# Kernel tuning notes

Hardware: AMD Instinct MI355X
Metric: run time of the kernel (lower is better)

The kernel has to match this reference:

```python
import jax, jax.numpy as jnp
import numpy as np

B, N, D, M = 8, 8192, 256, 2  # M from init_kwargs


def setup_inputs() -> dict:
    key = jax.random.key(0)
    ks = jax.random.split(key, 10)
    g_names = ['G_l_ii', 'G_l_ij', 'G_l_ji', 'G_l_jj', 'G_u_ii', 'G_u_ij', 'G_u_ji', 'G_u_jj']
    inp = {'input': jax.random.normal(ks[0], (B, N, D), dtype=jnp.float32)}
    for i, name in enumerate(g_names):
        inp[name] = jax.random.normal(ks[1 + i], (B, N - 1), dtype=jnp.float32)
    inp['Diag'] = jax.random.normal(ks[9], (B, N), dtype=jnp.float32)
    inp['transform'] = 1
    return inp


def _banded_sweep(x, a0, b0, lo, dm, hi, aL, bL):
    # One tridiagonal Givens sweep over axis 1 of x [B,N,D].
    # row 0:       a0*x[0]   + b0*x[1]
    # rows 1..N-2: lo*x[i-1] + dm*x[i] + hi*x[i+1]
    # row N-1:     aL*x[N-2] + bL*x[N-1]
    n = x.shape[1]
    y0 = a0[:, None, None] * x[:, 0:1] + b0[:, None, None] * x[:, 1:2]
    ym = (lo[:, :, None] * x[:, :-2]
          + dm[:, :, None] * x[:, 1:n - 1]
          + hi[:, :, None] * x[:, 2:])
    yl = aL[:, None, None] * x[:, n - 2:n - 1] + bL[:, None, None] * x[:, n - 1:n]
    return jnp.concatenate([y0, ym, yl], axis=1)


def _forward(x, gl_ii, gl_ij, gl_ji, gl_jj, gu_ii, gu_ij, gu_ji, gu_jj, diag, transform):
    b, n, d = x.shape
    if transform:
        # stride permutation (only defined for even N in the original)
        x = x.reshape(b, n // M, M, d).transpose(0, 2, 1, 3).reshape(b, n, d)
    else:
        x = diag[:, :, None] * x
    # upper sweep -> Y
    y = _banded_sweep(
        x,
        gu_ii[:, 0], gu_ij[:, 0],
        gu_ji[:, :-1], gu_jj[:, :-1] * gu_ii[:, 1:], gu_jj[:, :-1] * gu_ij[:, 1:],
        gu_ji[:, n - 2], gu_jj[:, n - 2])
    # lower sweep -> Z
    z = _banded_sweep(
        y,
        gl_ii[:, 0], gl_ij[:, 0],
        gl_ii[:, 1:] * gl_ji[:, :-1], gl_ii[:, 1:] * gl_jj[:, :-1], gl_ij[:, 1:],
        gl_ji[:, n - 2], gl_jj[:, n - 2])
    if transform:
        z = diag[:, :, None] * z
    else:
        z = z.reshape(b, n // M, M, d).transpose(0, 2, 1, 3).reshape(b, n, d)
    return z


def reference(input, G_l_ii, G_l_ij, G_l_ji, G_l_jj, G_u_ii, G_u_ij, G_u_ji, G_u_jj, Diag, transform):
    return _forward(input, G_l_ii, G_l_ij, G_l_ji, G_l_jj,
                    G_u_ii, G_u_ij, G_u_ji, G_u_jj, Diag, transform)
```

## Files before the change

### kernel.cpp

```cpp
#include <hip/hip_runtime.h>

#define NN 8192
#define DD 256
#define NH (NN / 2)
#define BB 8
#define RPW 8
#define WPB 4
#define RPB (RPW * WPB)
#define SROWS (RPB + 4)
#define NBLK (BB * NN / RPB)
#define CPX (NBLK / 8)

__device__ __forceinline__ float4 f4_scale(float s, float4 v) {
    return make_float4(s * v.x, s * v.y, s * v.z, s * v.w);
}
__device__ __forceinline__ float4 f4_fma(float s, float4 v, float4 a) {
    return make_float4(fmaf(s, v.x, a.x), fmaf(s, v.y, a.y),
                       fmaf(s, v.z, a.z), fmaf(s, v.w, a.w));
}

__global__ __launch_bounds__(256) void dhhp_kernel(
    const float* __restrict__ x,
    const float* __restrict__ gl_ii, const float* __restrict__ gl_ij,
    const float* __restrict__ gl_ji, const float* __restrict__ gl_jj,
    const float* __restrict__ gu_ii, const float* __restrict__ gu_ij,
    const float* __restrict__ gu_ji, const float* __restrict__ gu_jj,
    const float* __restrict__ diag, const int* __restrict__ transform,
    float* __restrict__ out)
{
    __shared__ float smem[SROWS * DD];

    const int bid = blockIdx.x;
    const int swz = (bid & 7) * CPX + (bid >> 3);
    const int b   = swz >> 8;
    const int j0b = (swz & 255) << 5;
    const int w   = __builtin_amdgcn_readfirstlane(threadIdx.x >> 6);
    const int col = (threadIdx.x & 63) << 2;
    const int tr  = *transform;

    const float* xb  = x    + (size_t)b * NN * DD;
    const float* db  = diag + (size_t)b * NN;
    const float* uii = gu_ii + (size_t)b * (NN - 1);
    const float* uij = gu_ij + (size_t)b * (NN - 1);
    const float* uji = gu_ji + (size_t)b * (NN - 1);
    const float* ujj = gu_jj + (size_t)b * (NN - 1);
    const float* lii = gl_ii + (size_t)b * (NN - 1);
    const float* lij = gl_ij + (size_t)b * (NN - 1);
    const float* lji = gl_ji + (size_t)b * (NN - 1);
    const float* ljj = gl_jj + (size_t)b * (NN - 1);
    float* ob = out + (size_t)b * NN * DD;

    #pragma unroll
    for (int q = 0; q < SROWS / WPB; ++q) {
        const int s  = w + q * WPB;
        const int i  = j0b - 2 + s;
        const int ic = i < 0 ? 0 : (i > NN - 1 ? NN - 1 : i);
        const int r  = tr ? ((ic < NH) ? (ic << 1) : (((ic - NH) << 1) | 1)) : ic;
        const float* gp = xb + (size_t)r * DD + col;
        float*       lp = smem + s * DD;
        __builtin_amdgcn_global_load_lds(
            (const __attribute__((address_space(1))) void*)gp,
            (__attribute__((address_space(3))) void*)lp, 16, 0, 0);
    }
    __syncthreads();

    const int j0 = j0b + (w << 3);

    auto xRow = [&](int i) -> float4 {
        const int s = i - (j0b - 2);
        float4 v = *reinterpret_cast<const float4*>(smem + s * DD + col);
        if (!tr) {
            const int ic = i < 0 ? 0 : (i > NN - 1 ? NN - 1 : i);
            v = f4_scale(db[ic], v);
        }
        return v;
    };
    auto yInner = [&](int i, float4 xm, float4 xc, float4 xp) -> float4 {
        float lo  = uji[i - 1];
        float cjj = ujj[i - 1];
        float dm  = cjj * uii[i];
        float hi  = cjj * uij[i];
        float4 r = f4_scale(lo, xm);
        r = f4_fma(dm, xc, r);
        r = f4_fma(hi, xp, r);
        return r;
    };
    auto yAny = [&](int i, float4 xm, float4 xc, float4 xp) -> float4 {
        int ic = i < 0 ? 0 : (i > NN - 1 ? NN - 1 : i);
        if (ic == 0)      return f4_fma(uii[0], xc, f4_scale(uij[0], xp));
        if (ic == NN - 1) return f4_fma(uji[NN - 2], xm, f4_scale(ujj[NN - 2], xc));
        return yInner(ic, xm, xc, xp);
    };
    auto zInner = [&](int j, float4 ym, float4 yc, float4 yp) -> float4 {
        float ci = lii[j];
        float lo = ci * lji[j - 1];
        float dm = ci * ljj[j - 1];
        float hi = lij[j];
        float4 r = f4_scale(lo, ym);
        r = f4_fma(dm, yc, r);
        r = f4_fma(hi, yp, r);
        return r;
    };
    auto zAny = [&](int j, float4 ym, float4 yc, float4 yp) -> float4 {
        if (j == 0)      return f4_fma(lii[0], yc, f4_scale(lij[0], yp));
        if (j == NN - 1) return f4_fma(lji[NN - 2], ym, f4_scale(ljj[NN - 2], yc));
        return zInner(j, ym, yc, yp);
    };
    auto storeRow = [&](int j, float4 z) {
        int jo;
        float4 o;
        if (tr) { o = f4_scale(db[j], z); jo = j; }
        else    { o = z; jo = (j & 1) ? (NH + (j >> 1)) : (j >> 1); }
        *reinterpret_cast<float4*>(ob + (size_t)jo * DD + col) = o;
    };

    float4 xr[RPW + 4];
    float4 yr[RPW + 2];

    const bool interior = (j0 >= 2) && (j0 <= NN - RPW - 2);

    if (interior) {
        #pragma unroll
        for (int t = 0; t < RPW + 4; ++t) xr[t] = xRow(j0 - 2 + t);
        #pragma unroll
        for (int t = 0; t < RPW + 2; ++t)
            yr[t] = yInner(j0 - 1 + t, xr[t], xr[t + 1], xr[t + 2]);
        #pragma unroll
        for (int t = 0; t < RPW; ++t)
            storeRow(j0 + t, zInner(j0 + t, yr[t], yr[t + 1], yr[t + 2]));
    } else {
        #pragma unroll
        for (int t = 0; t < RPW + 4; ++t) xr[t] = xRow(j0 - 2 + t);
        #pragma unroll
        for (int t = 0; t < RPW + 2; ++t)
            yr[t] = yAny(j0 - 1 + t, xr[t], xr[t + 1], xr[t + 2]);
        #pragma unroll
        for (int t = 0; t < RPW; ++t)
            storeRow(j0 + t, zAny(j0 + t, yr[t], yr[t + 1], yr[t + 2]));
    }
}

extern "C" void kernel_launch(void* const* d_in, const int* in_sizes, int n_in,
                              void* d_out, int out_size, void* d_ws, size_t ws_size,
                              hipStream_t stream) {
    const float* x     = (const float*)d_in[0];
    const float* gl_ii = (const float*)d_in[1];
    const float* gl_ij = (const float*)d_in[2];
    const float* gl_ji = (const float*)d_in[3];
    const float* gl_jj = (const float*)d_in[4];
    const float* gu_ii = (const float*)d_in[5];
    const float* gu_ij = (const float*)d_in[6];
    const float* gu_ji = (const float*)d_in[7];
    const float* gu_jj = (const float*)d_in[8];
    const float* diag  = (const float*)d_in[9];
    const int* transform = (const int*)d_in[10];
    float* out = (float*)d_out;

    dim3 grid(NBLK);
    dim3 block(256);
    hipLaunchKernelGGL(dhhp_kernel, grid, block, 0, stream,
                       x, gl_ii, gl_ij, gl_ji, gl_jj,
                       gu_ii, gu_ij, gu_ji, gu_jj, diag, transform, out);
}
```

Baseline: 31.41 us.

## Process two row tiles per block with overlapped LDS staging via partial waitcnt

Each block now handles two 32-row tiles, issuing global-to-LDS loads for both up front into double-buffered shared memory. It then waits only for the first tile's loads (partial vmcnt) before computing it, so the second tile's loads overlap with the first tile's compute. This halves the grid and doubles LDS per block, which may reduce occupancy. It also relies on hand-counted vmcnt values being correct relative to the loads and stores the compiler emits.

Measured after the change: 38.67 us. +23.1%, slower.

```diff
diff --git a/kernel.cpp b/kernel.cpp
--- a/kernel.cpp
+++ b/kernel.cpp
@@ -6,9 +6,11 @@
 #define BB 8
 #define RPW 8
 #define WPB 4
-#define RPB (RPW * WPB)
-#define SROWS (RPB + 4)
-#define NBLK (BB * NN / RPB)
+#define RPT (RPW * WPB)
+#define TPB 2
+#define SROWS (RPT + 4)
+#define LPW (SROWS / WPB)
+#define NBLK (BB * NN / (RPT * TPB))
 #define CPX (NBLK / 8)
 
 __device__ __forceinline__ float4 f4_scale(float s, float4 v) {
@@ -28,12 +30,12 @@
     const float* __restrict__ diag, const int* __restrict__ transform,
     float* __restrict__ out)
 {
-    __shared__ float smem[SROWS * DD];
+    __shared__ float smem[TPB * SROWS * DD];
 
     const int bid = blockIdx.x;
     const int swz = (bid & 7) * CPX + (bid >> 3);
-    const int b   = swz >> 8;
-    const int j0b = (swz & 255) << 5;
+    const int b   = swz >> 7;
+    const int t0  = (swz & 127) << 6;
     const int w   = __builtin_amdgcn_readfirstlane(threadIdx.x >> 6);
     const int col = (threadIdx.x & 63) << 2;
     const int tr  = *transform;
@@ -50,94 +52,112 @@
     const float* ljj = gl_jj + (size_t)b * (NN - 1);
     float* ob = out + (size_t)b * NN * DD;
 
-    #pragma unroll
-    for (int q = 0; q < SROWS / WPB; ++q) {
-        const int s  = w + q * WPB;
-        const int i  = j0b - 2 + s;
-        const int ic = i < 0 ? 0 : (i > NN - 1 ? NN - 1 : i);
-        const int r  = tr ? ((ic < NH) ? (ic << 1) : (((ic - NH) << 1) | 1)) : ic;
-        const float* gp = xb + (size_t)r * DD + col;
-        float*       lp = smem + s * DD;
-        __builtin_amdgcn_global_load_lds(
-            (const __attribute__((address_space(1))) void*)gp,
-            (__attribute__((address_space(3))) void*)lp, 16, 0, 0);
-    }
-    __syncthreads();
-
-    const int j0 = j0b + (w << 3);
-
-    auto xRow = [&](int i) -> float4 {
-        const int s = i - (j0b - 2);
-        float4 v = *reinterpret_cast<const float4*>(smem + s * DD + col);
-        if (!tr) {
+    auto stageTile = [&](int tb, int buf) {
+        #pragma unroll
+        for (int q = 0; q < LPW; ++q) {
+            const int s  = w + q * WPB;
+            const int i  = tb - 2 + s;
             const int ic = i < 0 ? 0 : (i > NN - 1 ? NN - 1 : i);
-            v = f4_scale(db[ic], v);
+            const int r  = tr ? ((ic < NH) ? (ic << 1) : (((ic - NH) << 1) | 1)) : ic;
+            const float* gp = xb + (size_t)r * DD + col;
+            float*       lp = smem + (size_t)(buf * SROWS + s) * DD;
+            __builtin_amdgcn_global_load_lds(
+                (const __attribute__((address_space(1))) void*)gp,
+                (__attribute__((address_space(3))) void*)lp, 16, 0, 0);
         }
-        return v;
-    };
-    auto yInner = [&](int i, float4 xm, float4 xc, float4 xp) -> float4 {
-        float lo  = uji[i - 1];
-        float cjj = ujj[i - 1];
-        float dm  = cjj * uii[i];
-        float hi  = cjj * uij[i];
-        float4 r = f4_scale(lo, xm);
-        r = f4_fma(dm, xc, r);
-        r = f4_fma(hi, xp, r);
-        return r;
-    };
-    auto yAny = [&](int i, float4 xm, float4 xc, float4 xp) -> float4 {
-        int ic = i < 0 ? 0 : (i > NN - 1 ? NN - 1 : i);
-        if (ic == 0)      return f4_fma(uii[0], xc, f4_scale(uij[0], xp));
-        if (ic == NN - 1) return f4_fma(uji[NN - 2], xm, f4_scale(ujj[NN - 2], xc));
-        return yInner(ic, xm, xc, xp);
-    };
-    auto zInner = [&](int j, float4 ym, float4 yc, float4 yp) -> float4 {
-        float ci = lii[j];
-        float lo = ci * lji[j - 1];
-        float dm = ci * ljj[j - 1];
-        float hi = lij[j];
-        float4 r = f4_scale(lo, ym);
-        r = f4_fma(dm, yc, r);
-        r = f4_fma(hi, yp, r);
-        return r;
-    };
-    auto zAny = [&](int j, float4 ym, float4 yc, float4 yp) -> float4 {
-        if (j == 0)      return f4_fma(lii[0], yc, f4_scale(lij[0], yp));
-        if (j == NN - 1) return f4_fma(lji[NN - 2], ym, f4_scale(ljj[NN - 2], yc));
-        return zInner(j, ym, yc, yp);
-    };
-    auto storeRow = [&](int j, float4 z) {
-        int jo;
-        float4 o;
-        if (tr) { o = f4_scale(db[j], z); jo = j; }
-        else    { o = z; jo = (j & 1) ? (NH + (j >> 1)) : (j >> 1); }
-        *reinterpret_cast<float4*>(ob + (size_t)jo * DD + col) = o;
     };
 
-    float4 xr[RPW + 4];
-    float4 yr[RPW + 2];
+    auto computeTile = [&](int tb, int buf) {
+        const int j0 = tb + (w << 3);
+        const float* sb = smem + (size_t)buf * SROWS * DD;
 
-    const bool interior = (j0 >= 2) && (j0 <= NN - RPW - 2);
+        auto xRow = [&](int i) -> float4 {
+            const int s = i - (tb - 2);
+            float4 v = *reinterpret_cast<const float4*>(sb + (size_t)s * DD + col);
+            if (!tr) {
+                const int ic = i < 0 ? 0 : (i > NN - 1 ? NN - 1 : i);
+                v = f4_scale(db[ic], v);
+            }
+            return v;
+        };
+        auto yInner = [&](int i, float4 xm, float4 xc, float4 xp) -> float4 {
+            float lo  = uji[i - 1];
+            float cjj = ujj[i - 1];
+            float dm  = cjj * uii[i];
+            float hi  = cjj * uij[i];
+            float4 r = f4_scale(lo, xm);
+            r = f4_fma(dm, xc, r);
+            r = f4_fma(hi, xp, r);
+            return r;
+        };
+        auto yAny = [&](int i, float4 xm, float4 xc, float4 xp) -> float4 {
+            int ic = i < 0 ? 0 : (i > NN - 1 ? NN - 1 : i);
+            if (ic == 0)      return f4_fma(uii[0], xc, f4_scale(uij[0], xp));
+            if (ic == NN - 1) return f4_fma(uji[NN - 2], xm, f4_scale(ujj[NN - 2], xc));
+            return yInner(ic, xm, xc, xp);
+        };
+        auto zInner = [&](int j, float4 ym, float4 yc, float4 yp) -> float4 {
+            float ci = lii[j];
+            float lo = ci * lji[j - 1];
+            float dm = ci * ljj[j - 1];
+            float hi = lij[j];
+            float4 r = f4_scale(lo, ym);
+            r = f4_fma(dm, yc, r);
+            r = f4_fma(hi, yp, r);
+            return r;
+        };
+        auto zAny = [&](int j, float4 ym, float4 yc, float4 yp) -> float4 {
+            if (j == 0)      return f4_fma(lii[0], yc, f4_scale(lij[0], yp));
+            if (j == NN - 1) return f4_fma(lji[NN - 2], ym, f4_scale(ljj[NN - 2], yc));
+            return zInner(j, ym, yc, yp);
+        };
+        auto storeRow = [&](int j, float4 z) {
+            int jo;
+            float4 o;
+            if (tr) { o = f4_scale(db[j], z); jo = j; }
+            else    { o = z; jo = (j & 1) ? (NH + (j >> 1)) : (j >> 1); }
+            *reinterpret_cast<float4*>(ob + (size_t)jo * DD + col) = o;
+        };
 
-    if (interior) {
-        #pragma unroll
-        for (int t = 0; t < RPW + 4; ++t) xr[t] = xRow(j0 - 2 + t);
-        #pragma unroll
-        for (int t = 0; t < RPW + 2; ++t)
-            yr[t] = yInner(j0 - 1 + t, xr[t], xr[t + 1], xr[t + 2]);
-        #pragma unroll
-        for (int t = 0; t < RPW; ++t)
-            storeRow(j0 + t, zInner(j0 + t, yr[t], yr[t + 1], yr[t + 2]));
-    } else {
-        #pragma unroll
-        for (int t = 0; t < RPW + 4; ++t) xr[t] = xRow(j0 - 2 + t);
-        #pragma unroll
-        for (int t = 0; t < RPW + 2; ++t)
-            yr[t] = yAny(j0 - 1 + t, xr[t], xr[t + 1], xr[t + 2]);
-        #pragma unroll
-        for (int t = 0; t < RPW; ++t)
-            storeRow(j0 + t, zAny(j0 + t, yr[t], yr[t + 1], yr[t + 2]));
-    }
+        float4 xr[RPW + 4];
+        float4 yr[RPW + 2];
+        const bool interior = (j0 >= 2) && (j0 <= NN - RPW - 2);
+
+        if (interior) {
+            #pragma unroll
+            for (int t = 0; t < RPW + 4; ++t) xr[t] = xRow(j0 - 2 + t);
+            #pragma unroll
+            for (int t = 0; t < RPW + 2; ++t)
+                yr[t] = yInner(j0 - 1 + t, xr[t], xr[t + 1], xr[t + 2]);
+            #pragma unroll
+            for (int t = 0; t < RPW; ++t)
+                storeRow(j0 + t, zInner(j0 + t, yr[t], yr[t + 1], yr[t + 2]));
+        } else {
+            #pragma unroll
+            for (int t = 0; t < RPW + 4; ++t) xr[t] = xRow(j0 - 2 + t);
+            #pragma unroll
+            for (int t = 0; t < RPW + 2; ++t)
+                yr[t] = yAny(j0 - 1 + t, xr[t], xr[t + 1], xr[t + 2]);
+            #pragma unroll
+            for (int t = 0; t < RPW; ++t)
+                storeRow(j0 + t, zAny(j0 + t, yr[t], yr[t + 1], yr[t + 2]));
+        }
+    };
+
+    stageTile(t0, 0);
+    stageTile(t0 + RPT, 1);
+
+    asm volatile("s_waitcnt vmcnt(9)" ::: "memory");
+    __builtin_amdgcn_sched_barrier(0);
+    __builtin_amdgcn_s_barrier();
+
+    computeTile(t0, 0);
+
+    asm volatile("s_waitcnt vmcnt(8)" ::: "memory");
+    __builtin_amdgcn_sched_barrier(0);
+    __builtin_amdgcn_s_barrier();
+
+    computeTile(t0 + RPT, 1);
 }
 
 extern "C" void kernel_launch(void* const* d_in, const int* in_sizes, int n_in,
```
